# Performance work log

Measured on AMD Instinct MI355X. Metric: run time of the kernel, lower is better.

Reference implementation:

```python
import jax, jax.numpy as jnp
import numpy as np

B, S, D, H = 2, 2048, 1024, 16
HD = D // H  # head_dim = 64


def setup_inputs() -> dict:
    key = jax.random.key(0)
    ks = jax.random.split(key, 12)
    scale = 1.0 / np.sqrt(D)
    inp = {
        "query": jax.random.normal(ks[0], (B, S, D), jnp.float32),
        "key": jax.random.normal(ks[1], (B, S, D), jnp.float32),
        "value": jax.random.normal(ks[2], (B, S, D), jnp.float32),
        # causal mask, broadcast over batch and heads; masked_fill where mask == 0
        "mask": jnp.tril(jnp.ones((1, 1, S, S), dtype=bool)),
        "Wq": jax.random.normal(ks[3], (D, D), jnp.float32) * scale,
        "bq": jax.random.normal(ks[4], (D,), jnp.float32) * scale,
        "Wk": jax.random.normal(ks[5], (D, D), jnp.float32) * scale,
        "bk": jax.random.normal(ks[6], (D,), jnp.float32) * scale,
        "Wv": jax.random.normal(ks[7], (D, D), jnp.float32) * scale,
        "bv": jax.random.normal(ks[8], (D,), jnp.float32) * scale,
        "Wo": jax.random.normal(ks[9], (D, D), jnp.float32) * scale,
        "bo": jax.random.normal(ks[10], (D,), jnp.float32) * scale,
    }
    return inp


def reference(query, key, value, mask, Wq, bq, Wk, bk, Wv, bv, Wo, bo):
    b = query.shape[0]
    # QKV projections -> [B, H, S, HD]
    q = (query @ Wq + bq).reshape(b, -1, H, HD).transpose(0, 2, 1, 3)
    k = (key @ Wk + bk).reshape(b, -1, H, HD).transpose(0, 2, 1, 3)
    v = (value @ Wv + bv).reshape(b, -1, H, HD).transpose(0, 2, 1, 3)
    # scores: [B, H, Sq, Sk]
    scores = jnp.einsum("bhqd,bhkd->bhqk", q, k) / jnp.sqrt(jnp.float32(HD))
    scores = jnp.where(mask, scores, jnp.float32(-1e9))
    attn = jax.nn.softmax(scores, axis=-1)
    # dropout is identity in eval mode
    ctx = jnp.einsum("bhqk,bhkd->bhqd", attn, v)  # [B, H, Sq, HD]
    concat = ctx.transpose(0, 2, 1, 3).reshape(b, -1, D)
    return concat @ Wo + bo
```

## Files before the change

### kernel.cpp

```cpp
#include <hip/hip_runtime.h>

#define B_ 2
#define S_ 2048
#define D_ 1024
#define H_ 16
#define HD_ 64
#define Msz (B_*S_)

typedef __attribute__((ext_vector_type(8))) short  short8v;
typedef __attribute__((ext_vector_type(4))) float  float4v;
typedef __attribute__((ext_vector_type(4))) unsigned int uint4v;

__device__ static __forceinline__ unsigned short f2bf(float x) {
    union { float f; unsigned u; } v; v.f = x;
    unsigned r = v.u + 0x7fffu + ((v.u >> 16) & 1u);
    return (unsigned short)(r >> 16);
}
__device__ static __forceinline__ float bf2f(unsigned short b) {
    union { float f; unsigned u; } v; v.u = ((unsigned)b) << 16;
    return v.f;
}
__device__ static __forceinline__ void split2(float x, unsigned short& hi, unsigned short& lo) {
    hi = f2bf(x);
    lo = f2bf(x - bf2f(hi));
}

__device__ static __forceinline__ void gl_lds16(const void* g, void* l) {
    __builtin_amdgcn_global_load_lds(
        (const __attribute__((address_space(1))) void*)g,
        (__attribute__((address_space(3))) void*)l, 16, 0, 0);
}

__global__ __launch_bounds__(256) void conv_split(
    const float* __restrict__ in, unsigned short* __restrict__ hi,
    unsigned short* __restrict__ lo, int n4)
{
    const int i = blockIdx.x * 256 + threadIdx.x;
    if (i >= n4) return;
    const float4 x = ((const float4*)in)[i];
    ushort4 h, l;
    split2(x.x, h.x, l.x);
    split2(x.y, h.y, l.y);
    split2(x.z, h.z, l.z);
    split2(x.w, h.w, l.w);
    ((ushort4*)hi)[i] = h;
    ((ushort4*)lo)[i] = l;
}

__global__ __launch_bounds__(256) void conv_split_T(
    const float* __restrict__ W, unsigned short* __restrict__ thi,
    unsigned short* __restrict__ tlo, int R, int C)
{
    __shared__ float t[32][33];
    const int tid = threadIdx.x;
    const int r8 = tid >> 5, c = tid & 31;
    const int kbase = blockIdx.y * 32;
    const int nbase = blockIdx.x * 32;
#pragma unroll
    for (int i = 0; i < 4; ++i)
        t[r8 + i*8][c] = W[(size_t)(kbase + r8 + i*8) * C + nbase + c];
    __syncthreads();
#pragma unroll
    for (int i = 0; i < 4; ++i) {
        const int rr = r8 + i*8;
        const float v = t[c][rr];
        unsigned short h, l; split2(v, h, l);
        thi[(size_t)(nbase + rr) * R + kbase + c] = h;
        tlo[(size_t)(nbase + rr) * R + kbase + c] = l;
    }
}

__global__ __launch_bounds__(512) void gemm3(
    const unsigned short* __restrict__ Aphi, const unsigned short* __restrict__ Aplo,
    const unsigned short* __restrict__ Bthi, const unsigned short* __restrict__ Btlo,
    const float* __restrict__ bias, float* __restrict__ out,
    unsigned short* __restrict__ ohi, unsigned short* __restrict__ olo,
    int M, int N, int K, int mode, float scale)
{
    __shared__ __align__(16) unsigned short Ah[128][64], Al[128][64];
    __shared__ __align__(16) unsigned short Bh[128][64], Bl[128][64];

    const int tid  = threadIdx.x;
    const int lane = tid & 63;
    const int w    = tid >> 6;
    const int wr = w >> 2, wc = w & 3;
    const int m0 = blockIdx.x * 128, n0 = blockIdx.y * 128;

    float4v acc[4][2];
#pragma unroll
    for (int mi = 0; mi < 4; ++mi)
#pragma unroll
        for (int ni = 0; ni < 2; ++ni)
#pragma unroll
            for (int r = 0; r < 4; ++r) acc[mi][ni][r] = 0.f;

    const int fr   = lane & 15;
    const int fk   = (lane >> 4) * 8;
    const int xorE = (lane & 7) * 8;
    const int srow = lane >> 3;
    const int sxor = ((lane & 7) ^ srow) * 8;

    const int bufsel = w >> 1;
    const int gbase  = (w & 1) * 8;

    for (int k0 = 0; k0 < K; k0 += 64) {
#pragma unroll
        for (int i = 0; i < 8; ++i) {
            const int row0 = (gbase + i) * 8;
            const int grow = row0 + srow;
            if (bufsel == 0)
                gl_lds16(&Aphi[(size_t)(m0+grow)*K + k0 + sxor], &Ah[row0][0]);
            else if (bufsel == 1)
                gl_lds16(&Aplo[(size_t)(m0+grow)*K + k0 + sxor], &Al[row0][0]);
            else if (bufsel == 2)
                gl_lds16(&Bthi[(size_t)(n0+grow)*K + k0 + sxor], &Bh[row0][0]);
            else
                gl_lds16(&Btlo[(size_t)(n0+grow)*K + k0 + sxor], &Bl[row0][0]);
        }
        __syncthreads();

#pragma unroll
        for (int ks = 0; ks < 2; ++ks) {
            short8v af[4][2], bf[2][2];
#pragma unroll
            for (int mi = 0; mi < 4; ++mi) {
                const int row = wr*64 + mi*16 + fr;
                af[mi][0] = *(const short8v*)&Ah[row][(ks*32 + fk) ^ xorE];
                af[mi][1] = *(const short8v*)&Al[row][(ks*32 + fk) ^ xorE];
            }
#pragma unroll
            for (int ni = 0; ni < 2; ++ni) {
                const int row = wc*32 + ni*16 + fr;
                bf[ni][0] = *(const short8v*)&Bh[row][(ks*32 + fk) ^ xorE];
                bf[ni][1] = *(const short8v*)&Bl[row][(ks*32 + fk) ^ xorE];
            }
#pragma unroll
            for (int mi = 0; mi < 4; ++mi)
#pragma unroll
                for (int ni = 0; ni < 2; ++ni) {
                    acc[mi][ni] = __builtin_amdgcn_mfma_f32_16x16x32_bf16(af[mi][0], bf[ni][0], acc[mi][ni], 0, 0, 0);
                    acc[mi][ni] = __builtin_amdgcn_mfma_f32_16x16x32_bf16(af[mi][0], bf[ni][1], acc[mi][ni], 0, 0, 0);
                    acc[mi][ni] = __builtin_amdgcn_mfma_f32_16x16x32_bf16(af[mi][1], bf[ni][0], acc[mi][ni], 0, 0, 0);
                }
        }
        __syncthreads();
    }

    const int rbase = (lane >> 4) * 4, cidx = lane & 15;
#pragma unroll
    for (int mi = 0; mi < 4; ++mi)
#pragma unroll
        for (int ni = 0; ni < 2; ++ni) {
            const int col = n0 + wc*32 + ni*16 + cidx;
            const float bv = bias[col];
#pragma unroll
            for (int r = 0; r < 4; ++r) {
                const int row = m0 + wr*64 + mi*16 + rbase + r;
                const float v = (acc[mi][ni][r] + bv) * scale;
                if (mode == 0) {
                    out[(size_t)row * N + col] = v;
                } else {
                    const int bb = row >> 11;
                    const int ss = row & (S_ - 1);
                    const int hh = col >> 6;
                    const int hd = col & (HD_ - 1);
                    const size_t o = (((size_t)(bb*H_ + hh) * S_) + ss) * HD_ + hd;
                    unsigned short hb, lb; split2(v, hb, lb);
                    ohi[o] = hb;
                    olo[o] = lb;
                }
            }
        }
}

__global__ __launch_bounds__(256) void transpose_v(
    const unsigned short* __restrict__ V, unsigned short* __restrict__ Vt)
{
    __shared__ unsigned tbuf[64][33];
    const int tid = threadIdx.x;
    const int head = blockIdx.y;
    const int s0 = blockIdx.x * 64;
    const unsigned short* src = V + (size_t)head * S_ * HD_;
    unsigned short* dst = Vt + (size_t)head * HD_ * S_;

    const int sp = tid >> 3;
    const int dch = tid & 7;
    const short8v a = *(const short8v*)&src[(size_t)(s0 + 2*sp    ) * HD_ + dch*8];
    const short8v b = *(const short8v*)&src[(size_t)(s0 + 2*sp + 1) * HD_ + dch*8];
#pragma unroll
    for (int j = 0; j < 8; ++j) {
        const unsigned lo = (unsigned short)a[j];
        const unsigned hi = (unsigned short)b[j];
        tbuf[dch*8 + j][sp] = lo | (hi << 16);
    }
    __syncthreads();
#pragma unroll
    for (int i = 0; i < 2; ++i) {
        const int c = i*256 + tid;
        const int d = c >> 3, ch = c & 7;
        uint4v o;
#pragma unroll
        for (int k = 0; k < 4; ++k) o[k] = tbuf[d][ch*4 + k];
        *(uint4v*)&dst[(size_t)d * S_ + s0 + ch*8] = o;
    }
}

__global__ __launch_bounds__(256) void attn_mfma(
    const unsigned short* __restrict__ Qhi, const unsigned short* __restrict__ Qlo,
    const unsigned short* __restrict__ Khi, const unsigned short* __restrict__ Klo,
    const unsigned short* __restrict__ Vt,
    unsigned short* __restrict__ Chi, unsigned short* __restrict__ Clo)
{
    __shared__ unsigned short Ks[2][2][64][64];
    __shared__ unsigned short Vs[2][64][64];
    __shared__ unsigned short Ps[4][32][64];

    const int tid = threadIdx.x, lane = tid & 63, w = tid >> 6;
    const int bid = blockIdx.x;
    const int head = bid & 31;
    const int qb = ((bid >> 5) + head) & 15;
    const int q0 = qb * 128;

    const size_t hQK = (size_t)head * S_ * HD_;
    const unsigned short* Qh = Qhi + hQK;
    const unsigned short* Ql = Qlo + hQK;
    const unsigned short* Kh = Khi + hQK;
    const unsigned short* Kl = Klo + hQK;
    const unsigned short* Vth = Vt + (size_t)head * HD_ * S_;

    const int fr = lane & 15;
    const int fk = (lane >> 4) * 8;
    const int xorE = (lane & 7) * 8;
    const int rbase = (lane >> 4) * 4;

    short8v qf[2][2][2];
#pragma unroll
    for (int mi = 0; mi < 2; ++mi)
#pragma unroll
        for (int ks = 0; ks < 2; ++ks) {
            const size_t off = (size_t)(q0 + w*32 + mi*16 + fr) * HD_ + ks*32 + fk;
            qf[mi][ks][0] = *(const short8v*)&Qh[off];
            qf[mi][ks][1] = *(const short8v*)&Ql[off];
        }

    float4v oacc[2][4];
#pragma unroll
    for (int mi = 0; mi < 2; ++mi)
#pragma unroll
        for (int dt = 0; dt < 4; ++dt)
#pragma unroll
            for (int r = 0; r < 4; ++r) oacc[mi][dt][r] = 0.f;
    float m_run[2][4], l_run[2][4];
#pragma unroll
    for (int mi = 0; mi < 2; ++mi)
#pragma unroll
        for (int r = 0; r < 4; ++r) { m_run[mi][r] = -3.0e38f; l_run[mi][r] = 0.f; }

    const int srow = lane >> 3;
    const int sxor = ((lane & 7) ^ srow) * 8;

    const int ntiles = 2*qb + 2;
    const int last_t = 2*qb + (w >> 1);

    auto stage = [&](int t, int buf) {
#pragma unroll
        for (int cc = 0; cc < 6; ++cc) {
            const int c = w*6 + cc;
            if (c < 8) {
                gl_lds16(&Kh[(size_t)(t*64 + c*8 + srow)*HD_ + sxor], &Ks[buf][0][c*8][0]);
            } else if (c < 16) {
                const int c2 = c - 8;
                gl_lds16(&Kl[(size_t)(t*64 + c2*8 + srow)*HD_ + sxor], &Ks[buf][1][c2*8][0]);
            } else {
                const int c2 = c - 16;
                gl_lds16(&Vth[(size_t)(c2*8 + srow)*S_ + t*64 + sxor], &Vs[buf][c2*8][0]);
            }
        }
    };

    stage(0, 0);
    int buf = 0;
    for (int t = 0; t < ntiles; ++t) {
        if (t + 1 < ntiles) {
            stage(t + 1, buf ^ 1);
            asm volatile("s_waitcnt vmcnt(6)" ::: "memory");
        } else {
            asm volatile("s_waitcnt vmcnt(0)" ::: "memory");
        }
        __builtin_amdgcn_s_barrier();
        __builtin_amdgcn_sched_barrier(0);

        if (t <= last_t) {
            float4v sacc[2][4];
#pragma unroll
            for (int mi = 0; mi < 2; ++mi)
#pragma unroll
                for (int ni = 0; ni < 4; ++ni)
#pragma unroll
                    for (int r = 0; r < 4; ++r) sacc[mi][ni][r] = 0.f;
#pragma unroll
            for (int ks = 0; ks < 2; ++ks)
#pragma unroll
                for (int ni = 0; ni < 4; ++ni) {
                    const short8v kh = *(const short8v*)&Ks[buf][0][ni*16 + fr][(ks*32 + fk) ^ xorE];
                    const short8v kl = *(const short8v*)&Ks[buf][1][ni*16 + fr][(ks*32 + fk) ^ xorE];
#pragma unroll
                    for (int mi = 0; mi < 2; ++mi) {
                        sacc[mi][ni] = __builtin_amdgcn_mfma_f32_16x16x32_bf16(qf[mi][ks][0], kh, sacc[mi][ni], 0, 0, 0);
                        sacc[mi][ni] = __builtin_amdgcn_mfma_f32_16x16x32_bf16(qf[mi][ks][1], kh, sacc[mi][ni], 0, 0, 0);
                        sacc[mi][ni] = __builtin_amdgcn_mfma_f32_16x16x32_bf16(qf[mi][ks][0], kl, sacc[mi][ni], 0, 0, 0);
                    }
                }

            const int kvb = t*64;
            if (kvb + 63 > q0 + w*32) {
#pragma unroll
                for (int mi = 0; mi < 2; ++mi)
#pragma unroll
                    for (int ni = 0; ni < 4; ++ni)
#pragma unroll
                        for (int r = 0; r < 4; ++r) {
                            const int row_g = q0 + w*32 + mi*16 + rbase + r;
                            const int col_g = kvb + ni*16 + fr;
                            if (col_g > row_g) sacc[mi][ni][r] = -1.0e9f;
                        }
            }

            float tmax[2][4];
#pragma unroll
            for (int mi = 0; mi < 2; ++mi)
#pragma unroll
                for (int r = 0; r < 4; ++r)
                    tmax[mi][r] = fmaxf(fmaxf(sacc[mi][0][r], sacc[mi][1][r]),
                                        fmaxf(sacc[mi][2][r], sacc[mi][3][r]));
#pragma unroll
            for (int d = 1; d <= 8; d <<= 1)
#pragma unroll
                for (int mi = 0; mi < 2; ++mi)
#pragma unroll
                    for (int r = 0; r < 4; ++r)
                        tmax[mi][r] = fmaxf(tmax[mi][r], __shfl_xor(tmax[mi][r], d, 64));
#pragma unroll
            for (int mi = 0; mi < 2; ++mi)
#pragma unroll
                for (int r = 0; r < 4; ++r) {
                    const float mnew = fmaxf(m_run[mi][r], tmax[mi][r]);
                    const float sc = __expf(m_run[mi][r] - mnew);
                    m_run[mi][r] = mnew;
                    l_run[mi][r] *= sc;
#pragma unroll
                    for (int dt = 0; dt < 4; ++dt) oacc[mi][dt][r] *= sc;
                }
#pragma unroll
            for (int mi = 0; mi < 2; ++mi)
#pragma unroll
                for (int ni = 0; ni < 4; ++ni)
#pragma unroll
                    for (int r = 0; r < 4; ++r) {
                        const float p = __expf(sacc[mi][ni][r] - m_run[mi][r]);
                        const unsigned short pb = f2bf(p);
                        l_run[mi][r] += bf2f(pb);
                        const int R = mi*16 + rbase + r;
                        Ps[w][R][(ni*16 + fr) ^ ((R & 7) * 8)] = pb;
                    }

#pragma unroll
            for (int ks = 0; ks < 2; ++ks) {
                short8v pa[2];
#pragma unroll
                for (int mi = 0; mi < 2; ++mi)
                    pa[mi] = *(const short8v*)&Ps[w][mi*16 + fr][(ks*32 + fk) ^ xorE];
#pragma unroll
                for (int dt = 0; dt < 4; ++dt) {
                    const short8v vf = *(const short8v*)&Vs[buf][dt*16 + fr][(ks*32 + fk) ^ xorE];
#pragma unroll
                    for (int mi = 0; mi < 2; ++mi)
                        oacc[mi][dt] = __builtin_amdgcn_mfma_f32_16x16x32_bf16(pa[mi], vf, oacc[mi][dt], 0, 0, 0);
                }
            }
        }

        __builtin_amdgcn_s_barrier();
        buf ^= 1;
    }

#pragma unroll
    for (int d = 1; d <= 8; d <<= 1)
#pragma unroll
        for (int mi = 0; mi < 2; ++mi)
#pragma unroll
            for (int r = 0; r < 4; ++r)
                l_run[mi][r] += __shfl_xor(l_run[mi][r], d, 64);

    const int b = head >> 4, h = head & 15;
#pragma unroll
    for (int mi = 0; mi < 2; ++mi)
#pragma unroll
        for (int r = 0; r < 4; ++r) {
            const float inv = 1.0f / l_run[mi][r];
            const int sg = q0 + w*32 + mi*16 + rbase + r;
            const size_t rb = ((size_t)(b * S_ + sg)) * D_ + h * 64;
#pragma unroll
            for (int dt = 0; dt < 4; ++dt) {
                const float v = oacc[mi][dt][r] * inv;
                unsigned short hb, lb; split2(v, hb, lb);
                Chi[rb + dt*16 + fr] = hb;
                Clo[rb + dt*16 + fr] = lb;
            }
        }
}

extern "C" void kernel_launch(void* const* d_in, const int* in_sizes, int n_in,
                              void* d_out, int out_size, void* d_ws, size_t ws_size,
                              hipStream_t stream)
{
    const float* query = (const float*)d_in[0];
    const float* key   = (const float*)d_in[1];
    const float* value = (const float*)d_in[2];
    const float* Wq = (const float*)d_in[4];
    const float* bq = (const float*)d_in[5];
    const float* Wk = (const float*)d_in[6];
    const float* bk = (const float*)d_in[7];
    const float* Wv = (const float*)d_in[8];
    const float* bv = (const float*)d_in[9];
    const float* Wo = (const float*)d_in[10];
    const float* bo = (const float*)d_in[11];
    float* out = (float*)d_out;

    const size_t nElem = (size_t)B_ * S_ * D_;
    char* wsb = (char*)d_ws;
    unsigned short* Xhi = (unsigned short*)(wsb + 0);
    unsigned short* Xlo = (unsigned short*)(wsb + 8ull*1024*1024);
    unsigned short* Qph = (unsigned short*)(wsb + 16ull*1024*1024);
    unsigned short* Qpl = (unsigned short*)(wsb + 24ull*1024*1024);
    unsigned short* Kph = (unsigned short*)(wsb + 32ull*1024*1024);
    unsigned short* Kpl = (unsigned short*)(wsb + 40ull*1024*1024);
    unsigned short* Vph = (unsigned short*)(wsb + 48ull*1024*1024);
    unsigned short* Vpl = (unsigned short*)(wsb + 56ull*1024*1024);
    unsigned short* Wph = (unsigned short*)(wsb + 64ull*1024*1024);
    unsigned short* Wpl = (unsigned short*)(wsb + 66ull*1024*1024);
    unsigned short* VtT = Xhi;
    unsigned short* Chi = Vph;
    unsigned short* Clo = Vpl;

    const dim3 cblk(256);
    const dim3 gblk(512);
    const dim3 cgrd(nElem / 1024);
    const dim3 tgrd(D_/32, D_/32);
    const dim3 ggrd(Msz/128, D_/128);
    const dim3 vtgrd(S_/64, B_*H_);
    const dim3 agrd(B_ * H_ * (S_/128));

    const float iscale = 0.125f;

    conv_split<<<cgrd, cblk, 0, stream>>>(query, Xhi, Xlo, (int)(nElem/4));
    conv_split_T<<<tgrd, cblk, 0, stream>>>(Wq, Wph, Wpl, D_, D_);
    gemm3<<<ggrd, gblk, 0, stream>>>(Xhi, Xlo, Wph, Wpl, bq, nullptr, Qph, Qpl, Msz, D_, D_, 1, iscale);
    conv_split<<<cgrd, cblk, 0, stream>>>(key, Xhi, Xlo, (int)(nElem/4));
    conv_split_T<<<tgrd, cblk, 0, stream>>>(Wk, Wph, Wpl, D_, D_);
    gemm3<<<ggrd, gblk, 0, stream>>>(Xhi, Xlo, Wph, Wpl, bk, nullptr, Kph, Kpl, Msz, D_, D_, 1, 1.0f);
    conv_split<<<cgrd, cblk, 0, stream>>>(value, Xhi, Xlo, (int)(nElem/4));
    conv_split_T<<<tgrd, cblk, 0, stream>>>(Wv, Wph, Wpl, D_, D_);
    gemm3<<<ggrd, gblk, 0, stream>>>(Xhi, Xlo, Wph, Wpl, bv, nullptr, Vph, Vpl, Msz, D_, D_, 1, 1.0f);
    transpose_v<<<vtgrd, cblk, 0, stream>>>(Vph, VtT);
    attn_mfma<<<agrd, cblk, 0, stream>>>(Qph, Qpl, Kph, Kpl, VtT, Chi, Clo);
    conv_split_T<<<tgrd, cblk, 0, stream>>>(Wo, Wph, Wpl, D_, D_);
    gemm3<<<ggrd, gblk, 0, stream>>>(Chi, Clo, Wph, Wpl, bo, out, nullptr, nullptr, Msz, D_, D_, 0, 1.0f);
}
```

Before: 447.9 us.

## Double-buffer LDS tiles in split-bf16 GEMM and remap block order

The projection GEMM now loads K-tiles of 32 into two ping-pong LDS buffers and issues the next tile's global-to-LDS copy before computing the current one. This overlaps memory latency with MFMA work and drops one barrier per iteration. It also uses a new XOR swizzle for the 32-wide rows and a 1D grid where consecutive blocks sweep N first, so blocks running together share A rows in cache. In exchange there are twice as many loop iterations over smaller K steps, and correctness depends on the async LDS writes being complete when the single barrier is reached.

```diff
diff --git a/kernel.cpp b/kernel.cpp
--- a/kernel.cpp
+++ b/kernel.cpp
@@ -70,21 +70,23 @@
     }
 }
 
-__global__ __launch_bounds__(512) void gemm3(
+__global__ __launch_bounds__(512) void gemm4(
     const unsigned short* __restrict__ Aphi, const unsigned short* __restrict__ Aplo,
     const unsigned short* __restrict__ Bthi, const unsigned short* __restrict__ Btlo,
     const float* __restrict__ bias, float* __restrict__ out,
     unsigned short* __restrict__ ohi, unsigned short* __restrict__ olo,
     int M, int N, int K, int mode, float scale)
 {
-    __shared__ __align__(16) unsigned short Ah[128][64], Al[128][64];
-    __shared__ __align__(16) unsigned short Bh[128][64], Bl[128][64];
+    __shared__ __align__(16) unsigned short Ah[2][128][32], Al[2][128][32];
+    __shared__ __align__(16) unsigned short Bh[2][128][32], Bl[2][128][32];
 
     const int tid  = threadIdx.x;
     const int lane = tid & 63;
     const int w    = tid >> 6;
     const int wr = w >> 2, wc = w & 3;
-    const int m0 = blockIdx.x * 128, n0 = blockIdx.y * 128;
+    const int bid = blockIdx.x;
+    const int m0 = (bid >> 3) * 128;
+    const int n0 = (bid & 7) * 128;
 
     float4v acc[4][2];
 #pragma unroll
@@ -95,55 +97,62 @@
             for (int r = 0; r < 4; ++r) acc[mi][ni][r] = 0.f;
 
     const int fr   = lane & 15;
-    const int fk   = (lane >> 4) * 8;
-    const int xorE = (lane & 7) * 8;
-    const int srow = lane >> 3;
-    const int sxor = ((lane & 7) ^ srow) * 8;
-
-    const int bufsel = w >> 1;
-    const int gbase  = (w & 1) * 8;
-
-    for (int k0 = 0; k0 < K; k0 += 64) {
-#pragma unroll
-        for (int i = 0; i < 8; ++i) {
-            const int row0 = (gbase + i) * 8;
-            const int grow = row0 + srow;
-            if (bufsel == 0)
-                gl_lds16(&Aphi[(size_t)(m0+grow)*K + k0 + sxor], &Ah[row0][0]);
-            else if (bufsel == 1)
-                gl_lds16(&Aplo[(size_t)(m0+grow)*K + k0 + sxor], &Al[row0][0]);
-            else if (bufsel == 2)
-                gl_lds16(&Bthi[(size_t)(n0+grow)*K + k0 + sxor], &Bh[row0][0]);
-            else
-                gl_lds16(&Btlo[(size_t)(n0+grow)*K + k0 + sxor], &Bl[row0][0]);
-        }
+    const int kch  = lane >> 4;
+    const int rco  = ((kch ^ ((fr >> 2) & 3)) * 8);
+    const int sr16 = lane >> 2;
+    const int sch  = ((lane & 3) ^ ((lane >> 4) & 3)) * 8;
+
+    const int tsel = w >> 1;
+    const int half = (w & 1) * 64;
+
+    const unsigned short* tp =
+        (tsel == 0) ? Aphi : (tsel == 1) ? Aplo : (tsel == 2) ? Bthi : Btlo;
+    const int base0 = (tsel < 2) ? m0 : n0;
+
+    auto STAGE = [&](int kb, int t) {
+        const int k0 = t * 32;
+#pragma unroll
+        for (int i = 0; i < 4; ++i) {
+            const int row0 = half + i * 16;
+            const unsigned short* src = &tp[(size_t)(base0 + row0 + sr16) * K + k0 + sch];
+            unsigned short* dst =
+                (tsel == 0) ? &Ah[kb][row0][0] : (tsel == 1) ? &Al[kb][row0][0] :
+                (tsel == 2) ? &Bh[kb][row0][0] : &Bl[kb][row0][0];
+            gl_lds16(src, dst);
+        }
+    };
+
+    const int NT = K >> 5;
+    STAGE(0, 0);
+    __syncthreads();
+    int cur = 0;
+    for (int t = 0; t < NT; ++t) {
+        if (t + 1 < NT) STAGE(cur ^ 1, t + 1);
+
+        short8v af[4][2], bf[2][2];
+#pragma unroll
+        for (int mi = 0; mi < 4; ++mi) {
+            const int row = wr*64 + mi*16 + fr;
+            af[mi][0] = *(const short8v*)&Ah[cur][row][rco];
+            af[mi][1] = *(const short8v*)&Al[cur][row][rco];
+        }
+#pragma unroll
+        for (int ni = 0; ni < 2; ++ni) {
+            const int row = wc*32 + ni*16 + fr;
+            bf[ni][0] = *(const short8v*)&Bh[cur][row][rco];
+            bf[ni][1] = *(const short8v*)&Bl[cur][row][rco];
+        }
+#pragma unroll
+        for (int mi = 0; mi < 4; ++mi)
+#pragma unroll
+            for (int ni = 0; ni < 2; ++ni) {
+                acc[mi][ni] = __builtin_amdgcn_mfma_f32_16x16x32_bf16(af[mi][0], bf[ni][0], acc[mi][ni], 0, 0, 0);
+                acc[mi][ni] = __builtin_amdgcn_mfma_f32_16x16x32_bf16(af[mi][0], bf[ni][1], acc[mi][ni], 0, 0, 0);
+                acc[mi][ni] = __builtin_amdgcn_mfma_f32_16x16x32_bf16(af[mi][1], bf[ni][0], acc[mi][ni], 0, 0, 0);
+            }
+
         __syncthreads();
-
-#pragma unroll
-        for (int ks = 0; ks < 2; ++ks) {
-            short8v af[4][2], bf[2][2];
-#pragma unroll
-            for (int mi = 0; mi < 4; ++mi) {
-                const int row = wr*64 + mi*16 + fr;
-                af[mi][0] = *(const short8v*)&Ah[row][(ks*32 + fk) ^ xorE];
-                af[mi][1] = *(const short8v*)&Al[row][(ks*32 + fk) ^ xorE];
-            }
-#pragma unroll
-            for (int ni = 0; ni < 2; ++ni) {
-                const int row = wc*32 + ni*16 + fr;
-                bf[ni][0] = *(const short8v*)&Bh[row][(ks*32 + fk) ^ xorE];
-                bf[ni][1] = *(const short8v*)&Bl[row][(ks*32 + fk) ^ xorE];
-            }
-#pragma unroll
-            for (int mi = 0; mi < 4; ++mi)
-#pragma unroll
-                for (int ni = 0; ni < 2; ++ni) {
-                    acc[mi][ni] = __builtin_amdgcn_mfma_f32_16x16x32_bf16(af[mi][0], bf[ni][0], acc[mi][ni], 0, 0, 0);
-                    acc[mi][ni] = __builtin_amdgcn_mfma_f32_16x16x32_bf16(af[mi][0], bf[ni][1], acc[mi][ni], 0, 0, 0);
-                    acc[mi][ni] = __builtin_amdgcn_mfma_f32_16x16x32_bf16(af[mi][1], bf[ni][0], acc[mi][ni], 0, 0, 0);
-                }
-        }
-        __syncthreads();
+        cur ^= 1;
     }
 
     const int rbase = (lane >> 4) * 4, cidx = lane & 15;
@@ -447,7 +456,7 @@
     const dim3 gblk(512);
     const dim3 cgrd(nElem / 1024);
     const dim3 tgrd(D_/32, D_/32);
-    const dim3 ggrd(Msz/128, D_/128);
+    const dim3 ggrd((Msz/128) * (D_/128));
     const dim3 vtgrd(S_/64, B_*H_);
     const dim3 agrd(B_ * H_ * (S_/128));
 
@@ -455,15 +464,15 @@
 
     conv_split<<<cgrd, cblk, 0, stream>>>(query, Xhi, Xlo, (int)(nElem/4));
     conv_split_T<<<tgrd, cblk, 0, stream>>>(Wq, Wph, Wpl, D_, D_);
-    gemm3<<<ggrd, gblk, 0, stream>>>(Xhi, Xlo, Wph, Wpl, bq, nullptr, Qph, Qpl, Msz, D_, D_, 1, iscale);
+    gemm4<<<ggrd, gblk, 0, stream>>>(Xhi, Xlo, Wph, Wpl, bq, nullptr, Qph, Qpl, Msz, D_, D_, 1, iscale);
     conv_split<<<cgrd, cblk, 0, stream>>>(key, Xhi, Xlo, (int)(nElem/4));
     conv_split_T<<<tgrd, cblk, 0, stream>>>(Wk, Wph, Wpl, D_, D_);
-    gemm3<<<ggrd, gblk, 0, stream>>>(Xhi, Xlo, Wph, Wpl, bk, nullptr, Kph, Kpl, Msz, D_, D_, 1, 1.0f);
+    gemm4<<<ggrd, gblk, 0, stream>>>(Xhi, Xlo, Wph, Wpl, bk, nullptr, Kph, Kpl, Msz, D_, D_, 1, 1.0f);
     conv_split<<<cgrd, cblk, 0, stream>>>(value, Xhi, Xlo, (int)(nElem/4));
     conv_split_T<<<tgrd, cblk, 0, stream>>>(Wv, Wph, Wpl, D_, D_);
-    gemm3<<<ggrd, gblk, 0, stream>>>(Xhi, Xlo, Wph, Wpl, bv, nullptr, Vph, Vpl, Msz, D_, D_, 1, 1.0f);
+    gemm4<<<ggrd, gblk, 0, stream>>>(Xhi, Xlo, Wph, Wpl, bv, nullptr, Vph, Vpl, Msz, D_, D_, 1, 1.0f);
     transpose_v<<<vtgrd, cblk, 0, stream>>>(Vph, VtT);
     attn_mfma<<<agrd, cblk, 0, stream>>>(Qph, Qpl, Kph, Kpl, VtT, Chi, Clo);
     conv_split_T<<<tgrd, cblk, 0, stream>>>(Wo, Wph, Wpl, D_, D_);
-    gemm3<<<ggrd, gblk, 0, stream>>>(Chi, Clo, Wph, Wpl, bo, out, nullptr, nullptr, Msz, D_, D_, 0, 1.0f);
-}
+    gemm4<<<ggrd, gblk, 0, stream>>>(Chi, Clo, Wph, Wpl, bo, out, nullptr, nullptr, Msz, D_, D_, 0, 1.0f);
+}
```

New measurement: 432.9 us. 3.3% less time.
